# Performance work log

Measured on AMD Instinct MI355X. Metric: run time of the kernel, lower is better.

Reference implementation:

```python
import jax, jax.numpy as jnp
import numpy as np
from jax import lax

# pywt db4 decomposition lowpass filter
_DEC_LO_NP = np.array([-0.010597401784997278, 0.032883011666982945,
                        0.030841381835986965, -0.18703481171888114,
                        -0.02798376941698385, 0.6308807679295904,
                        0.7148465705525415, 0.23037781330885523], dtype=np.float32)
_SIGNS = np.array([(-1.0) ** (k + 1) for k in range(8)], dtype=np.float32)
DEC_LO = jnp.asarray(_DEC_LO_NP)                    # dec_lo
DEC_HI = jnp.asarray(_DEC_LO_NP[::-1] * _SIGNS)     # dec_hi (QMF)
LF = 8
MAX_LEVEL = 4
# analysis kernels: torch cross-correlates with reversed dec filters == true conv
H_ANA = jnp.stack([DEC_LO[::-1], DEC_HI[::-1]])[:, None, :]  # (2,1,LF)
# synthesis: torch conv_transpose with rec filters == xcorr(dilated x, flip(rec)) = xcorr with dec
G0F = DEC_LO[None, None, :]
G1F = DEC_HI[None, None, :]
DN = ('NCH', 'OIH', 'NCH')


def _dwt_step(x):
    # x: (N, Lx) -> (lo, hi) each (N, outsize); pytorch_wavelets afb1d, mode='symmetric'
    N = x.shape[-1]
    outsize = (N + LF - 1) // 2          # pywt.dwt_coeff_len
    p = 2 * (outsize - 1) - N + LF
    xp = jnp.pad(x, ((0, 0), (p // 2, (p + 1) // 2)), mode='symmetric')
    y = lax.conv_general_dilated(xp[:, None, :], H_ANA, (2,), 'VALID',
                                 dimension_numbers=DN)  # (N,2,outsize)
    return y[:, 0, :], y[:, 1, :]


def _idwt_step(lo, hi):
    # pytorch_wavelets sfb1d: conv_transpose(stride=2, padding=LF-2)
    # == lhs-dilated xcorr with flipped rec filters (= dec filters), pad 1 each side
    y0 = lax.conv_general_dilated(lo[:, None, :], G0F, (1,), [(1, 1)],
                                  lhs_dilation=(2,), dimension_numbers=DN)
    y1 = lax.conv_general_dilated(hi[:, None, :], G1F, (1,), [(1, 1)],
                                  lhs_dilation=(2,), dimension_numbers=DN)
    return (y0 + y1)[:, 0, :]            # (N, 2*Llo + 2 - LF)


def dywpe(x, proj_w, proj_b, scale_emb, gate_w, gate_b):
    B, L, _ = x.shape
    d_model = scale_emb.shape[1]
    # channel_proj -> mono signal (B, L)
    x_mono = (jnp.einsum('blc,oc->blo', x, proj_w) + proj_b)[..., 0]
    # multi-level DWT
    lo = x_mono
    highs = []
    for _ in range(MAX_LEVEL):
        lo, hi = _dwt_step(lo)
        highs.append(hi)
    # gates: sigmoid(g) * tanh(v), per scale -> (MAX_LEVEL+1, d_model)
    gated = scale_emb @ gate_w.T + gate_b
    g, v = jnp.split(gated, 2, axis=-1)
    gates = jax.nn.sigmoid(g) * jnp.tanh(v)

    def mod(coef, gate):  # (B,Lc) x (d,) -> (B*d, Lc): outer product, fold d into batch
        return (coef[:, None, :] * gate[None, :, None]).reshape(B * d_model, -1)

    x0 = mod(lo, gates[0])
    hs = [mod(highs[i], gates[i + 1]) for i in range(MAX_LEVEL)]
    # IDWT, coarsest level first
    for h in hs[::-1]:
        if x0.shape[-1] > h.shape[-1]:
            x0 = x0[:, :h.shape[-1]]
        x0 = _idwt_step(x0, h)
    pe = x0.reshape(B, d_model, -1).transpose(0, 2, 1)  # (B, L', d_model)
    if pe.shape[1] < L:
        pe = jnp.pad(pe, ((0, 0), (0, L - pe.shape[1]), (0, 0)))
    elif pe.shape[1] > L:
        pe = pe[:, :L]
    return pe


def setup_inputs() -> dict:
    key = jax.random.key(0)
    ks = jax.random.split(key, 6)
    B, L, d_x, d_model, J = 32, 4096, 8, 512, 4
    return {
        'x': jax.random.normal(ks[0], (B, L, d_x), dtype=jnp.float32),
        'proj_w': jax.random.normal(ks[1], (1, d_x), dtype=jnp.float32) * 0.3,
        'proj_b': jax.random.normal(ks[2], (1,), dtype=jnp.float32) * 0.02,
        'scale_emb': jax.random.normal(ks[3], (J + 1, d_model), dtype=jnp.float32),
        'gate_w': jax.random.normal(ks[4], (2 * d_model, d_model), dtype=jnp.float32) * 0.04,
        'gate_b': jax.random.normal(ks[5], (2 * d_model,), dtype=jnp.float32) * 0.02,
    }


def reference(x, proj_w, proj_b, scale_emb, gate_w, gate_b):
    return dywpe(x, proj_w, proj_b, scale_emb, gate_w, gate_b)
```

## Files before the change

kernel.cpp:

```cpp
#include <hip/hip_runtime.h>

#define NB   32
#define LSEQ 4096
#define DM   512

typedef float f32x4 __attribute__((ext_vector_type(4)));

__device__ __constant__ float c_DL[8] = {
    -0.010597401784997278f,  0.032883011666982945f,  0.030841381835986965f,
    -0.18703481171888114f,  -0.02798376941698385f,   0.6308807679295904f,
     0.7148465705525415f,    0.23037781330885523f};
__device__ __constant__ float c_DH[8] = {
    -0.23037781330885523f,   0.7148465705525415f,   -0.6308807679295904f,
    -0.02798376941698385f,   0.18703481171888114f,   0.030841381835986965f,
    -0.032883011666982945f, -0.010597401784997278f};

#define GATES_OFF 0
#define P_OFF     (5 * DM)
#define P_STRIDE  2052

__device__ __forceinline__ int reflect_idx(int i, int N) {
    if (i < 0)  i = -1 - i;
    if (i >= N) i = 2 * N - 1 - i;
    return i;
}

__device__ void fwd_step(const float* __restrict__ src, int N,
                         float* __restrict__ lo, float* __restrict__ hi) {
    int outsize = (N + 7) >> 1;
    int p = 2 * (outsize - 1) - N + 8;
    int padL = p >> 1;
    for (int t = threadIdx.x; t < outsize; t += blockDim.x) {
        int base = 2 * t - padL;
        float aL = 0.f, aH = 0.f;
#pragma unroll
        for (int k = 0; k < 8; ++k) {
            float xv = src[reflect_idx(base + k, N)];
            aL = fmaf(xv, c_DL[7 - k], aL);
            aH = fmaf(xv, c_DH[7 - k], aH);
        }
        lo[t] = aL;
        hi[t] = aH;
    }
}

template <bool HI>
__device__ void inv_step(const float* __restrict__ c, int n, float* __restrict__ y) {
    int outN = 2 * n - 6;
    for (int t = threadIdx.x; t < outN; t += blockDim.x) {
        int base = t >> 1;
        int odd = t & 1;
        float f0 = odd ? (HI ? c_DH[0] : c_DL[0]) : (HI ? c_DH[1] : c_DL[1]);
        float f1 = odd ? (HI ? c_DH[2] : c_DL[2]) : (HI ? c_DH[3] : c_DL[3]);
        float f2 = odd ? (HI ? c_DH[4] : c_DL[4]) : (HI ? c_DH[5] : c_DL[5]);
        float f3 = odd ? (HI ? c_DH[6] : c_DL[6]) : (HI ? c_DH[7] : c_DL[7]);
        float acc = c[base] * f0;
        acc = fmaf(c[base + 1], f1, acc);
        acc = fmaf(c[base + 2], f2, acc);
        acc = fmaf(c[base + 3], f3, acc);
        y[t] = acc;
    }
}

__global__ __launch_bounds__(1024) void prep_kernel(
    const float* __restrict__ x, const float* __restrict__ proj_w,
    const float* __restrict__ proj_b, const float* __restrict__ scale_emb,
    const float* __restrict__ gate_w, const float* __restrict__ gate_b,
    float* __restrict__ ws) {
    if (blockIdx.x >= NB) {
        int lane = threadIdx.x & 63;
        int c = (blockIdx.x - NB) * 16 + (threadIdx.x >> 6);
        const float4* rg = (const float4*)(gate_w + (size_t)c * DM) + lane * 2;
        const float4* rv = (const float4*)(gate_w + (size_t)(c + DM) * DM) + lane * 2;
        float4 a0 = rg[0], a1 = rg[1];
        float4 b0 = rv[0], b1 = rv[1];
        float gacc[5], vacc[5];
#pragma unroll
        for (int j = 0; j < 5; ++j) {
            const float4* sj = (const float4*)(scale_emb + (size_t)j * DM) + lane * 2;
            float4 s0 = sj[0], s1 = sj[1];
            float ga;
            ga = s0.x * a0.x;            ga = fmaf(s0.y, a0.y, ga);
            ga = fmaf(s0.z, a0.z, ga);   ga = fmaf(s0.w, a0.w, ga);
            ga = fmaf(s1.x, a1.x, ga);   ga = fmaf(s1.y, a1.y, ga);
            ga = fmaf(s1.z, a1.z, ga);   ga = fmaf(s1.w, a1.w, ga);
            float va;
            va = s0.x * b0.x;            va = fmaf(s0.y, b0.y, va);
            va = fmaf(s0.z, b0.z, va);   va = fmaf(s0.w, b0.w, va);
            va = fmaf(s1.x, b1.x, va);   va = fmaf(s1.y, b1.y, va);
            va = fmaf(s1.z, b1.z, va);   va = fmaf(s1.w, b1.w, va);
            gacc[j] = ga;
            vacc[j] = va;
        }
#pragma unroll
        for (int j = 0; j < 5; ++j) {
#pragma unroll
            for (int off = 32; off > 0; off >>= 1) {
                gacc[j] += __shfl_xor(gacc[j], off, 64);
                vacc[j] += __shfl_xor(vacc[j], off, 64);
            }
        }
        if (lane == 0) {
            float bg = gate_b[c], bv = gate_b[DM + c];
#pragma unroll
            for (int j = 0; j < 5; ++j) {
                float g = gacc[j] + bg;
                float v = vacc[j] + bv;
                float sg = 1.f / (1.f + expf(-g));
                ws[GATES_OFF + j * DM + c] = sg * tanhf(v);
            }
        }
        return;
    }

    __shared__ float A[4096];
    __shared__ float Bb[2052];
    __shared__ float H2[1029];
    __shared__ float H3[518];
    __shared__ float H4[262];
    __shared__ float L4[262];
    __shared__ float C0a[518],  C4a[518];
    __shared__ float C0b[1030], C4b[1030], C3[1030];

    int b = blockIdx.x;
    float* P = ws + P_OFF;

    float w[8];
#pragma unroll
    for (int k = 0; k < 8; ++k) w[k] = proj_w[k];
    float pb = proj_b[0];

    const float* xb = x + (size_t)b * LSEQ * 8;
    for (int l = threadIdx.x; l < LSEQ; l += blockDim.x) {
        const float4* xv = (const float4*)(xb + (size_t)l * 8);
        float4 a0 = xv[0], a1 = xv[1];
        float acc = pb;
        acc = fmaf(a0.x, w[0], acc); acc = fmaf(a0.y, w[1], acc);
        acc = fmaf(a0.z, w[2], acc); acc = fmaf(a0.w, w[3], acc);
        acc = fmaf(a1.x, w[4], acc); acc = fmaf(a1.y, w[5], acc);
        acc = fmaf(a1.z, w[6], acc); acc = fmaf(a1.w, w[7], acc);
        A[l] = acc;
    }
    __syncthreads();

    fwd_step(A, 4096, Bb, P + (size_t)(1 * NB + b) * P_STRIDE);  __syncthreads();
    fwd_step(Bb, 2051, A, H2);  __syncthreads();
    fwd_step(A, 1029, Bb, H3);  __syncthreads();
    fwd_step(Bb, 518, L4, H4);  __syncthreads();

    inv_step<false>(L4, 262, C0a);
    inv_step<true >(H4, 262, C4a);
    inv_step<true >(H3, 518, C3);
    inv_step<true >(H2, 1029, P + (size_t)(2 * NB + b) * P_STRIDE);
    __syncthreads();
    inv_step<false>(C0a, 518, C0b);
    inv_step<false>(C4a, 518, C4b);
    inv_step<false>(C3, 1029, P + (size_t)(3 * NB + b) * P_STRIDE);
    __syncthreads();
    inv_step<false>(C0b, 1029, P + (size_t)(0 * NB + b) * P_STRIDE);
    inv_step<false>(C4b, 1029, P + (size_t)(4 * NB + b) * P_STRIDE);
}

__global__ __launch_bounds__(256) void expand_kernel(
    const float* __restrict__ ws, float* __restrict__ out) {
    const float* gates = ws + GATES_OFF;
    __shared__ float gl[5 * DM];
    __shared__ float sArr[5 * 32];
    for (int i = threadIdx.x; i < 5 * DM / 4; i += 256)
        ((float4*)gl)[i] = ((const float4*)gates)[i];

    int bid = blockIdx.x;
    int b  = bid >> 7;
    int l0 = (bid & 127) * 32;

    int t = threadIdx.x;
    if (t < 160) {
        int j = t >> 5, r = t & 31;
        int l = l0 + r;
        int base = l >> 1;
        int odd = l & 1;
        bool hi = (j == 1);
        const float* Pj = ws + P_OFF + (size_t)(j * NB + b) * P_STRIDE;
        float f0 = odd ? (hi ? c_DH[0] : c_DL[0]) : (hi ? c_DH[1] : c_DL[1]);
        float f1 = odd ? (hi ? c_DH[2] : c_DL[2]) : (hi ? c_DH[3] : c_DL[3]);
        float f2 = odd ? (hi ? c_DH[4] : c_DL[4]) : (hi ? c_DH[5] : c_DL[5]);
        float f3 = odd ? (hi ? c_DH[6] : c_DL[6]) : (hi ? c_DH[7] : c_DL[7]);
        float acc = Pj[base] * f0;
        acc = fmaf(Pj[base + 1], f1, acc);
        acc = fmaf(Pj[base + 2], f2, acc);
        acc = fmaf(Pj[base + 3], f3, acc);
        sArr[t] = acc;
    }
    __syncthreads();

    int half = threadIdx.x >> 7;
    int c4 = threadIdx.x & 127;
    float4 g0 = ((const float4*)(gl + 0 * DM))[c4];
    float4 g1 = ((const float4*)(gl + 1 * DM))[c4];
    float4 g2 = ((const float4*)(gl + 2 * DM))[c4];
    float4 g3 = ((const float4*)(gl + 3 * DM))[c4];
    float4 g4 = ((const float4*)(gl + 4 * DM))[c4];

#pragma unroll 4
    for (int r = 0; r < 16; ++r) {
        int rr = r * 2 + half;
        int row = bid * 32 + rr;
        float s0 = sArr[rr];
        float s1 = sArr[32 + rr];
        float s2 = sArr[64 + rr];
        float s3 = sArr[96 + rr];
        float s4 = sArr[128 + rr];
        f32x4 acc;
        acc.x = fmaf(s4, g4.x, fmaf(s3, g3.x, fmaf(s2, g2.x, fmaf(s1, g1.x, s0 * g0.x))));
        acc.y = fmaf(s4, g4.y, fmaf(s3, g3.y, fmaf(s2, g2.y, fmaf(s1, g1.y, s0 * g0.y))));
        acc.z = fmaf(s4, g4.z, fmaf(s3, g3.z, fmaf(s2, g2.z, fmaf(s1, g1.z, s0 * g0.z))));
        acc.w = fmaf(s4, g4.w, fmaf(s3, g3.w, fmaf(s2, g2.w, fmaf(s1, g1.w, s0 * g0.w))));
        __builtin_nontemporal_store(acc, (f32x4*)out + (size_t)row * (DM / 4) + c4);
    }
}

extern "C" void kernel_launch(void* const* d_in, const int* in_sizes, int n_in,
                              void* d_out, int out_size, void* d_ws, size_t ws_size,
                              hipStream_t stream) {
    const float* x         = (const float*)d_in[0];
    const float* proj_w    = (const float*)d_in[1];
    const float* proj_b    = (const float*)d_in[2];
    const float* scale_emb = (const float*)d_in[3];
    const float* gate_w    = (const float*)d_in[4];
    const float* gate_b    = (const float*)d_in[5];
    float* out = (float*)d_out;
    float* ws  = (float*)d_ws;

    prep_kernel<<<NB + DM / 16, 1024, 0, stream>>>(x, proj_w, proj_b,
                                                   scale_emb, gate_w, gate_b, ws);
    expand_kernel<<<(NB * LSEQ) / 32, 256, 0, stream>>>(ws, out);
}
```

Measured before the change: 68.05 us.

## Fuse wavelet transform into expand kernel with per-chunk halo recomputation

Replaces the per-batch serial DWT/IDWT prep blocks (32 blocks of 1024 threads) and the global workspace of reconstructed coefficients with a fused kernel. Each 256-thread block recomputes only the windowed range of every wavelet level needed for its 64 output rows, using halos, and then writes the expanded output directly. The gates computation moves into its own small kernel. This removes the low-parallelism prep phase and the workspace round trip, at the cost of redundant halo computation and more syncthreads per block.

```diff
diff --git a/kernel.cpp b/kernel.cpp
--- a/kernel.cpp
+++ b/kernel.cpp
@@ -1,8 +1,10 @@
 #include <hip/hip_runtime.h>
 
-#define NB   32
-#define LSEQ 4096
-#define DM   512
+#define NB    32
+#define LSEQ  4096
+#define DM    512
+#define ROWS  64
+#define CHUNKS (LSEQ / ROWS)
 
 typedef float f32x4 __attribute__((ext_vector_type(4)));
 
@@ -15,9 +17,8 @@
     -0.02798376941698385f,   0.18703481171888114f,   0.030841381835986965f,
     -0.032883011666982945f, -0.010597401784997278f};
 
-#define GATES_OFF 0
-#define P_OFF     (5 * DM)
-#define P_STRIDE  2052
+__device__ __forceinline__ int imin(int a, int b) { return a < b ? a : b; }
+__device__ __forceinline__ int imax(int a, int b) { return a > b ? a : b; }
 
 __device__ __forceinline__ int reflect_idx(int i, int N) {
     if (i < 0)  i = -1 - i;
@@ -25,30 +26,26 @@
     return i;
 }
 
-__device__ void fwd_step(const float* __restrict__ src, int N,
-                         float* __restrict__ lo, float* __restrict__ hi) {
-    int outsize = (N + 7) >> 1;
-    int p = 2 * (outsize - 1) - N + 8;
-    int padL = p >> 1;
-    for (int t = threadIdx.x; t < outsize; t += blockDim.x) {
-        int base = 2 * t - padL;
-        float aL = 0.f, aH = 0.f;
+template <bool HI>
+__device__ void fwd_range(const float* __restrict__ src, int src_lo, int Nsrc,
+                          float* __restrict__ dst, int d_lo, int d_hi) {
+    for (int t = d_lo + (int)threadIdx.x; t <= d_hi; t += 256) {
+        int base = 2 * t - 6;
+        float acc = 0.f;
 #pragma unroll
         for (int k = 0; k < 8; ++k) {
-            float xv = src[reflect_idx(base + k, N)];
-            aL = fmaf(xv, c_DL[7 - k], aL);
-            aH = fmaf(xv, c_DH[7 - k], aH);
+            float xv = src[reflect_idx(base + k, Nsrc) - src_lo];
+            acc = fmaf(xv, HI ? c_DH[7 - k] : c_DL[7 - k], acc);
         }
-        lo[t] = aL;
-        hi[t] = aH;
+        dst[t - d_lo] = acc;
     }
 }
 
 template <bool HI>
-__device__ void inv_step(const float* __restrict__ c, int n, float* __restrict__ y) {
-    int outN = 2 * n - 6;
-    for (int t = threadIdx.x; t < outN; t += blockDim.x) {
-        int base = t >> 1;
+__device__ void inv_range(const float* __restrict__ c, int c_lo,
+                          float* __restrict__ y, int y_lo, int y_hi) {
+    for (int t = y_lo + (int)threadIdx.x; t <= y_hi; t += 256) {
+        int base = (t >> 1) - c_lo;
         int odd = t & 1;
         float f0 = odd ? (HI ? c_DH[0] : c_DL[0]) : (HI ? c_DH[1] : c_DL[1]);
         float f1 = odd ? (HI ? c_DH[2] : c_DL[2]) : (HI ? c_DH[3] : c_DL[3]);
@@ -58,129 +55,140 @@
         acc = fmaf(c[base + 1], f1, acc);
         acc = fmaf(c[base + 2], f2, acc);
         acc = fmaf(c[base + 3], f3, acc);
-        y[t] = acc;
-    }
-}
-
-__global__ __launch_bounds__(1024) void prep_kernel(
+        y[t - y_lo] = acc;
+    }
+}
+
+__global__ __launch_bounds__(1024) void gates_kernel(
+    const float* __restrict__ scale_emb, const float* __restrict__ gate_w,
+    const float* __restrict__ gate_b, float* __restrict__ gates) {
+    int lane = threadIdx.x & 63;
+    int c = blockIdx.x * 16 + (threadIdx.x >> 6);
+    const float4* rg = (const float4*)(gate_w + (size_t)c * DM) + lane * 2;
+    const float4* rv = (const float4*)(gate_w + (size_t)(c + DM) * DM) + lane * 2;
+    float4 a0 = rg[0], a1 = rg[1];
+    float4 b0 = rv[0], b1 = rv[1];
+    float gacc[5], vacc[5];
+#pragma unroll
+    for (int j = 0; j < 5; ++j) {
+        const float4* sj = (const float4*)(scale_emb + (size_t)j * DM) + lane * 2;
+        float4 s0 = sj[0], s1 = sj[1];
+        float ga;
+        ga = s0.x * a0.x;            ga = fmaf(s0.y, a0.y, ga);
+        ga = fmaf(s0.z, a0.z, ga);   ga = fmaf(s0.w, a0.w, ga);
+        ga = fmaf(s1.x, a1.x, ga);   ga = fmaf(s1.y, a1.y, ga);
+        ga = fmaf(s1.z, a1.z, ga);   ga = fmaf(s1.w, a1.w, ga);
+        float va;
+        va = s0.x * b0.x;            va = fmaf(s0.y, b0.y, va);
+        va = fmaf(s0.z, b0.z, va);   va = fmaf(s0.w, b0.w, va);
+        va = fmaf(s1.x, b1.x, va);   va = fmaf(s1.y, b1.y, va);
+        va = fmaf(s1.z, b1.z, va);   va = fmaf(s1.w, b1.w, va);
+        gacc[j] = ga;
+        vacc[j] = va;
+    }
+#pragma unroll
+    for (int j = 0; j < 5; ++j) {
+#pragma unroll
+        for (int off = 32; off > 0; off >>= 1) {
+            gacc[j] += __shfl_xor(gacc[j], off, 64);
+            vacc[j] += __shfl_xor(vacc[j], off, 64);
+        }
+    }
+    if (lane == 0) {
+        float bg = gate_b[c], bv = gate_b[DM + c];
+#pragma unroll
+        for (int j = 0; j < 5; ++j) {
+            float g = gacc[j] + bg;
+            float v = vacc[j] + bv;
+            float sg = 1.f / (1.f + expf(-g));
+            gates[j * DM + c] = sg * tanhf(v);
+        }
+    }
+}
+
+__global__ __launch_bounds__(256) void fused_kernel(
     const float* __restrict__ x, const float* __restrict__ proj_w,
-    const float* __restrict__ proj_b, const float* __restrict__ scale_emb,
-    const float* __restrict__ gate_w, const float* __restrict__ gate_b,
-    float* __restrict__ ws) {
-    if (blockIdx.x >= NB) {
-        int lane = threadIdx.x & 63;
-        int c = (blockIdx.x - NB) * 16 + (threadIdx.x >> 6);
-        const float4* rg = (const float4*)(gate_w + (size_t)c * DM) + lane * 2;
-        const float4* rv = (const float4*)(gate_w + (size_t)(c + DM) * DM) + lane * 2;
-        float4 a0 = rg[0], a1 = rg[1];
-        float4 b0 = rv[0], b1 = rv[1];
-        float gacc[5], vacc[5];
-#pragma unroll
-        for (int j = 0; j < 5; ++j) {
-            const float4* sj = (const float4*)(scale_emb + (size_t)j * DM) + lane * 2;
-            float4 s0 = sj[0], s1 = sj[1];
-            float ga;
-            ga = s0.x * a0.x;            ga = fmaf(s0.y, a0.y, ga);
-            ga = fmaf(s0.z, a0.z, ga);   ga = fmaf(s0.w, a0.w, ga);
-            ga = fmaf(s1.x, a1.x, ga);   ga = fmaf(s1.y, a1.y, ga);
-            ga = fmaf(s1.z, a1.z, ga);   ga = fmaf(s1.w, a1.w, ga);
-            float va;
-            va = s0.x * b0.x;            va = fmaf(s0.y, b0.y, va);
-            va = fmaf(s0.z, b0.z, va);   va = fmaf(s0.w, b0.w, va);
-            va = fmaf(s1.x, b1.x, va);   va = fmaf(s1.y, b1.y, va);
-            va = fmaf(s1.z, b1.z, va);   va = fmaf(s1.w, b1.w, va);
-            gacc[j] = ga;
-            vacc[j] = va;
-        }
-#pragma unroll
-        for (int j = 0; j < 5; ++j) {
-#pragma unroll
-            for (int off = 32; off > 0; off >>= 1) {
-                gacc[j] += __shfl_xor(gacc[j], off, 64);
-                vacc[j] += __shfl_xor(vacc[j], off, 64);
-            }
-        }
-        if (lane == 0) {
-            float bg = gate_b[c], bv = gate_b[DM + c];
-#pragma unroll
-            for (int j = 0; j < 5; ++j) {
-                float g = gacc[j] + bg;
-                float v = vacc[j] + bv;
-                float sg = 1.f / (1.f + expf(-g));
-                ws[GATES_OFF + j * DM + c] = sg * tanhf(v);
-            }
-        }
-        return;
-    }
-
-    __shared__ float A[4096];
-    __shared__ float Bb[2052];
-    __shared__ float H2[1029];
-    __shared__ float H3[518];
-    __shared__ float H4[262];
-    __shared__ float L4[262];
-    __shared__ float C0a[518],  C4a[518];
-    __shared__ float C0b[1030], C4b[1030], C3[1030];
-
-    int b = blockIdx.x;
-    float* P = ws + P_OFF;
-
+    const float* __restrict__ proj_b, const float* __restrict__ gates,
+    float* __restrict__ out) {
+    __shared__ float GL[5 * DM];
+    __shared__ float XW[288];
+    __shared__ float LO1[140], LO2[68], LO3[32];
+    __shared__ float HI1[36], H2W[24], H3W[16], L4W[12], H4W[12];
+    __shared__ float AW[16], A4W[16], A3W[24], BW[24], B4W[24];
+    __shared__ float P0W[36], P2W[36], P3W[36], P4W[36];
+    __shared__ float SJ[5 * ROWS];
+
+    int bid = blockIdx.x;
+    int b  = bid >> 6;
+    int l0 = (bid & 63) * ROWS;
+
+    int p0 = l0 >> 1,  p1 = ((l0 + ROWS - 1) >> 1) + 3;
+    int b0 = p0 >> 1,  b1 = (p1 >> 1) + 3;
+    int a0 = b0 >> 1,  a1 = (b1 >> 1) + 3;
+    int w0 = a0 >> 1,  w1 = (a1 >> 1) + 3;
+    int t3lo = imax(imin(imin(2 * w0 - 6, a0), 517), 0);
+    int t3hi = imin(imax(imax(2 * w1 + 1, a1), 0), 517);
+    int t2lo = imax(imin(2 * t3lo - 6, 2 * a0 - 6), 0);
+    int t2hi = imin(imax(2 * t3hi + 1, 2 * a1 + 1), 1028);
+    int t1lo = imax(imin(2 * t2lo - 6, 2 * b0 - 6), 0);
+    int t1hi = imin(imax(2 * t2hi + 1, 2 * b1 + 1), 2050);
+    int txlo = imax(imin(2 * t1lo - 6, 2 * p0 - 6), 0);
+    int txhi = imin(imax(2 * t1hi + 1, 2 * p1 + 1), 4095);
+
+    for (int i = threadIdx.x; i < 5 * DM / 4; i += 256)
+        ((f32x4*)GL)[i] = ((const f32x4*)gates)[i];
     float w[8];
 #pragma unroll
     for (int k = 0; k < 8; ++k) w[k] = proj_w[k];
     float pb = proj_b[0];
-
     const float* xb = x + (size_t)b * LSEQ * 8;
-    for (int l = threadIdx.x; l < LSEQ; l += blockDim.x) {
-        const float4* xv = (const float4*)(xb + (size_t)l * 8);
-        float4 a0 = xv[0], a1 = xv[1];
+    for (int i = txlo + (int)threadIdx.x; i <= txhi; i += 256) {
+        const float4* xv = (const float4*)(xb + (size_t)i * 8);
+        float4 q0 = xv[0], q1 = xv[1];
         float acc = pb;
-        acc = fmaf(a0.x, w[0], acc); acc = fmaf(a0.y, w[1], acc);
-        acc = fmaf(a0.z, w[2], acc); acc = fmaf(a0.w, w[3], acc);
-        acc = fmaf(a1.x, w[4], acc); acc = fmaf(a1.y, w[5], acc);
-        acc = fmaf(a1.z, w[6], acc); acc = fmaf(a1.w, w[7], acc);
-        A[l] = acc;
-    }
-    __syncthreads();
-
-    fwd_step(A, 4096, Bb, P + (size_t)(1 * NB + b) * P_STRIDE);  __syncthreads();
-    fwd_step(Bb, 2051, A, H2);  __syncthreads();
-    fwd_step(A, 1029, Bb, H3);  __syncthreads();
-    fwd_step(Bb, 518, L4, H4);  __syncthreads();
-
-    inv_step<false>(L4, 262, C0a);
-    inv_step<true >(H4, 262, C4a);
-    inv_step<true >(H3, 518, C3);
-    inv_step<true >(H2, 1029, P + (size_t)(2 * NB + b) * P_STRIDE);
-    __syncthreads();
-    inv_step<false>(C0a, 518, C0b);
-    inv_step<false>(C4a, 518, C4b);
-    inv_step<false>(C3, 1029, P + (size_t)(3 * NB + b) * P_STRIDE);
-    __syncthreads();
-    inv_step<false>(C0b, 1029, P + (size_t)(0 * NB + b) * P_STRIDE);
-    inv_step<false>(C4b, 1029, P + (size_t)(4 * NB + b) * P_STRIDE);
-}
-
-__global__ __launch_bounds__(256) void expand_kernel(
-    const float* __restrict__ ws, float* __restrict__ out) {
-    const float* gates = ws + GATES_OFF;
-    __shared__ float gl[5 * DM];
-    __shared__ float sArr[5 * 32];
-    for (int i = threadIdx.x; i < 5 * DM / 4; i += 256)
-        ((float4*)gl)[i] = ((const float4*)gates)[i];
-
-    int bid = blockIdx.x;
-    int b  = bid >> 7;
-    int l0 = (bid & 127) * 32;
-
-    int t = threadIdx.x;
-    if (t < 160) {
-        int j = t >> 5, r = t & 31;
+        acc = fmaf(q0.x, w[0], acc); acc = fmaf(q0.y, w[1], acc);
+        acc = fmaf(q0.z, w[2], acc); acc = fmaf(q0.w, w[3], acc);
+        acc = fmaf(q1.x, w[4], acc); acc = fmaf(q1.y, w[5], acc);
+        acc = fmaf(q1.z, w[6], acc); acc = fmaf(q1.w, w[7], acc);
+        XW[i - txlo] = acc;
+    }
+    __syncthreads();
+
+    fwd_range<false>(XW, txlo, 4096, LO1, t1lo, t1hi);
+    fwd_range<true >(XW, txlo, 4096, HI1, p0, p1);
+    __syncthreads();
+    fwd_range<false>(LO1, t1lo, 2051, LO2, t2lo, t2hi);
+    fwd_range<true >(LO1, t1lo, 2051, H2W, b0, b1);
+    __syncthreads();
+    fwd_range<false>(LO2, t2lo, 1029, LO3, t3lo, t3hi);
+    fwd_range<true >(LO2, t2lo, 1029, H3W, a0, a1);
+    __syncthreads();
+    fwd_range<false>(LO3, t3lo, 518, L4W, w0, w1);
+    fwd_range<true >(LO3, t3lo, 518, H4W, w0, w1);
+    __syncthreads();
+
+    inv_range<false>(L4W, w0, AW,  a0, a1);
+    inv_range<true >(H4W, w0, A4W, a0, a1);
+    inv_range<true >(H3W, a0, A3W, b0, b1);
+    inv_range<true >(H2W, b0, P2W, p0, p1);
+    __syncthreads();
+    inv_range<false>(AW,  a0, BW,  b0, b1);
+    inv_range<false>(A4W, a0, B4W, b0, b1);
+    inv_range<false>(A3W, b0, P3W, p0, p1);
+    __syncthreads();
+    inv_range<false>(BW,  b0, P0W, p0, p1);
+    inv_range<false>(B4W, b0, P4W, p0, p1);
+    __syncthreads();
+
+    for (int idx = threadIdx.x; idx < 5 * ROWS; idx += 256) {
+        int j = idx >> 6;
+        int r = idx & (ROWS - 1);
         int l = l0 + r;
-        int base = l >> 1;
+        int base = (l >> 1) - p0;
         int odd = l & 1;
+        const float* Pj = (j == 0) ? P0W : (j == 1) ? HI1 :
+                          (j == 2) ? P2W : (j == 3) ? P3W : P4W;
         bool hi = (j == 1);
-        const float* Pj = ws + P_OFF + (size_t)(j * NB + b) * P_STRIDE;
         float f0 = odd ? (hi ? c_DH[0] : c_DL[0]) : (hi ? c_DH[1] : c_DL[1]);
         float f1 = odd ? (hi ? c_DH[2] : c_DL[2]) : (hi ? c_DH[3] : c_DL[3]);
         float f2 = odd ? (hi ? c_DH[4] : c_DL[4]) : (hi ? c_DH[5] : c_DL[5]);
@@ -189,33 +197,33 @@
         acc = fmaf(Pj[base + 1], f1, acc);
         acc = fmaf(Pj[base + 2], f2, acc);
         acc = fmaf(Pj[base + 3], f3, acc);
-        sArr[t] = acc;
+        SJ[idx] = acc;
     }
     __syncthreads();
 
     int half = threadIdx.x >> 7;
     int c4 = threadIdx.x & 127;
-    float4 g0 = ((const float4*)(gl + 0 * DM))[c4];
-    float4 g1 = ((const float4*)(gl + 1 * DM))[c4];
-    float4 g2 = ((const float4*)(gl + 2 * DM))[c4];
-    float4 g3 = ((const float4*)(gl + 3 * DM))[c4];
-    float4 g4 = ((const float4*)(gl + 4 * DM))[c4];
-
+    f32x4 g0 = ((const f32x4*)(GL + 0 * DM))[c4];
+    f32x4 g1 = ((const f32x4*)(GL + 1 * DM))[c4];
+    f32x4 g2 = ((const f32x4*)(GL + 2 * DM))[c4];
+    f32x4 g3 = ((const f32x4*)(GL + 3 * DM))[c4];
+    f32x4 g4 = ((const f32x4*)(GL + 4 * DM))[c4];
+
+    size_t rowbase = (size_t)b * LSEQ + l0;
 #pragma unroll 4
-    for (int r = 0; r < 16; ++r) {
+    for (int r = 0; r < ROWS / 2; ++r) {
         int rr = r * 2 + half;
-        int row = bid * 32 + rr;
-        float s0 = sArr[rr];
-        float s1 = sArr[32 + rr];
-        float s2 = sArr[64 + rr];
-        float s3 = sArr[96 + rr];
-        float s4 = sArr[128 + rr];
+        float s0 = SJ[rr];
+        float s1 = SJ[64 + rr];
+        float s2 = SJ[128 + rr];
+        float s3 = SJ[192 + rr];
+        float s4 = SJ[256 + rr];
         f32x4 acc;
         acc.x = fmaf(s4, g4.x, fmaf(s3, g3.x, fmaf(s2, g2.x, fmaf(s1, g1.x, s0 * g0.x))));
         acc.y = fmaf(s4, g4.y, fmaf(s3, g3.y, fmaf(s2, g2.y, fmaf(s1, g1.y, s0 * g0.y))));
         acc.z = fmaf(s4, g4.z, fmaf(s3, g3.z, fmaf(s2, g2.z, fmaf(s1, g1.z, s0 * g0.z))));
         acc.w = fmaf(s4, g4.w, fmaf(s3, g3.w, fmaf(s2, g2.w, fmaf(s1, g1.w, s0 * g0.w))));
-        __builtin_nontemporal_store(acc, (f32x4*)out + (size_t)row * (DM / 4) + c4);
+        __builtin_nontemporal_store(acc, (f32x4*)out + (rowbase + rr) * (DM / 4) + c4);
     }
 }
 
@@ -228,10 +236,9 @@
     const float* scale_emb = (const float*)d_in[3];
     const float* gate_w    = (const float*)d_in[4];
     const float* gate_b    = (const float*)d_in[5];
-    float* out = (float*)d_out;
-    float* ws  = (float*)d_ws;
-
-    prep_kernel<<<NB + DM / 16, 1024, 0, stream>>>(x, proj_w, proj_b,
-                                                   scale_emb, gate_w, gate_b, ws);
-    expand_kernel<<<(NB * LSEQ) / 32, 256, 0, stream>>>(ws, out);
-}
+    float* out   = (float*)d_out;
+    float* gates = (float*)d_ws;
+
+    gates_kernel<<<32, 1024, 0, stream>>>(scale_emb, gate_w, gate_b, gates);
+    fused_kernel<<<NB * CHUNKS, 256, 0, stream>>>(x, proj_w, proj_b, gates, out);
+}
```

Measured after the change: 66.30 us. -2.6%, faster.
